# Performance work log

Hardware: AMD Instinct MI355X
Metric: run time of the kernel (lower is better)

Reference implementation:

```python
import jax, jax.numpy as jnp
import numpy as np

DIM = 1024
HEADS = 16
HEAD_DIM = DIM // HEADS
HIDDEN = 4 * DIM
B, N = 4, 2048


def _layernorm(x, g, b, eps=1e-5):
    mu = jnp.mean(x, axis=-1, keepdims=True)
    var = jnp.var(x, axis=-1, keepdims=True)
    return (x - mu) * jax.lax.rsqrt(var + eps) * g + b


def setup_inputs() -> dict:
    key = jax.random.key(0)
    ks = jax.random.split(key, 8)
    s_in = 1.0 / np.sqrt(DIM)
    s_hid = 1.0 / np.sqrt(HIDDEN)
    return {
        "x": jax.random.normal(ks[0], (B, N, DIM), jnp.float32),
        "w_qkv": jax.random.normal(ks[1], (DIM, 3 * DIM), jnp.float32) * s_in,
        "w_proj": jax.random.normal(ks[2], (DIM, DIM), jnp.float32) * s_in,
        "b_proj": jnp.zeros((DIM,), jnp.float32),
        "ln1_g": jnp.ones((DIM,), jnp.float32),
        "ln1_b": jnp.zeros((DIM,), jnp.float32),
        "w1": jax.random.normal(ks[3], (DIM, HIDDEN), jnp.float32) * s_in,
        "b1": jnp.zeros((HIDDEN,), jnp.float32),
        "w2": jax.random.normal(ks[4], (HIDDEN, DIM), jnp.float32) * s_hid,
        "b2": jnp.zeros((DIM,), jnp.float32),
        "ln2_g": jnp.ones((DIM,), jnp.float32),
        "ln2_b": jnp.zeros((DIM,), jnp.float32),
    }


def reference(x, w_qkv, w_proj, b_proj, ln1_g, ln1_b, w1, b1, w2, b2, ln2_g, ln2_b):
    # --- multi-head self-attention (pre-norm), dropout=0 (eval) ---
    h = _layernorm(x, ln1_g, ln1_b)
    qkv = h @ w_qkv                       # [B,N,3*DIM]
    qkv = qkv.reshape(B, N, 3, HEADS, HEAD_DIM)
    q = jnp.transpose(qkv[:, :, 0], (0, 2, 1, 3))  # [B,H,N,hd]
    k = jnp.transpose(qkv[:, :, 1], (0, 2, 1, 3))
    v = jnp.transpose(qkv[:, :, 2], (0, 2, 1, 3))
    scale = HEAD_DIM ** -0.5
    attn = jnp.einsum('bhqd,bhkd->bhqk', q, k) * scale  # [B,H,N,N]
    attn = jax.nn.softmax(attn, axis=-1)
    o = jnp.einsum('bhqk,bhkd->bhqd', attn, v)
    o = jnp.transpose(o, (0, 2, 1, 3)).reshape(B, N, DIM)
    x = o @ w_proj + b_proj + x
    # --- feed-forward (pre-norm), exact GELU ---
    h = _layernorm(x, ln2_g, ln2_b)
    h = jax.nn.gelu(h @ w1 + b1, approximate=False)
    return h @ w2 + b2 + x
```

## Files before the change

### kernel.cpp

```cpp
#include <hip/hip_runtime.h>
#include <cstdint>
#include <cstddef>

typedef float  v4f  __attribute__((ext_vector_type(4)));
typedef __bf16 v8bf __attribute__((ext_vector_type(8)));
typedef __bf16 v4bf __attribute__((ext_vector_type(4)));

__device__ __forceinline__ float b2f(unsigned short u) {
  union { unsigned int i; float f; } cv; cv.i = ((unsigned int)u) << 16; return cv.f;
}
__device__ __forceinline__ unsigned short f2b(float f) {
  union { float f; unsigned int i; } cv; cv.f = f;
  unsigned int i = cv.i;
  i += 0x7fffu + ((i >> 16) & 1u);
  return (unsigned short)(i >> 16);
}
__device__ __forceinline__ unsigned short f2b_trunc(float f) {
  union { float f; unsigned int i; } cv; cv.f = f;
  return (unsigned short)(cv.i >> 16);
}
__device__ __forceinline__ float gelu_fast(float x) {
  const float u = x * (1.5957691216f + 0.07135481627f * x * x);
  return x * (1.0f / (1.0f + __expf(-u)));
}
__device__ __forceinline__ void g2l16(const unsigned short* g, unsigned short* l) {
  __builtin_amdgcn_global_load_lds(
      (const __attribute__((address_space(1))) void*)g,
      (__attribute__((address_space(3))) void*)l,
      16, 0, 0);
}

__global__ __launch_bounds__(256) void transpose_k(const float* __restrict__ in,
                                                   unsigned short* __restrict__ out,
                                                   int R, int C) {
  __shared__ float tile[32][33];
  const int tx = threadIdx.x, ty = threadIdx.y;
  const int r0 = blockIdx.y * 32, c0 = blockIdx.x * 32;
#pragma unroll
  for (int j = 0; j < 4; ++j)
    tile[ty + 8 * j][tx] = in[(size_t)(r0 + ty + 8 * j) * C + c0 + tx];
  __syncthreads();
#pragma unroll
  for (int j = 0; j < 4; ++j)
    out[(size_t)(c0 + ty + 8 * j) * R + r0 + tx] = f2b(tile[tx][ty + 8 * j]);
}

__global__ __launch_bounds__(256) void ln_kernel(const void* __restrict__ xp, int in_bf16,
                                                 const float* __restrict__ g,
                                                 const float* __restrict__ bta,
                                                 unsigned short* __restrict__ out) {
  const int r = blockIdx.x, t = threadIdx.x;
  float v0, v1, v2, v3;
  if (in_bf16) {
    const ushort4 raw = *(const ushort4*)((const unsigned short*)xp + (size_t)r * 1024 + t * 4);
    v0 = b2f(raw.x); v1 = b2f(raw.y); v2 = b2f(raw.z); v3 = b2f(raw.w);
  } else {
    const float4 raw = *(const float4*)((const float*)xp + (size_t)r * 1024 + t * 4);
    v0 = raw.x; v1 = raw.y; v2 = raw.z; v3 = raw.w;
  }
  float s  = v0 + v1 + v2 + v3;
  float s2 = v0 * v0 + v1 * v1 + v2 * v2 + v3 * v3;
#pragma unroll
  for (int off = 32; off > 0; off >>= 1) {
    s  += __shfl_down(s, off);
    s2 += __shfl_down(s2, off);
  }
  __shared__ float red[8];
  const int w = t >> 6, lane = t & 63;
  if (lane == 0) { red[w] = s; red[4 + w] = s2; }
  __syncthreads();
  if (t == 0) {
    float ts = red[0] + red[1] + red[2] + red[3];
    float t2 = red[4] + red[5] + red[6] + red[7];
    float mu = ts * (1.0f / 1024.0f);
    float var = t2 * (1.0f / 1024.0f) - mu * mu;
    red[0] = mu;
    red[1] = rsqrtf(var + 1e-5f);
  }
  __syncthreads();
  const float mu = red[0], rs = red[1];
  const float4 graw = *(const float4*)(g + t * 4);
  const float4 braw = *(const float4*)(bta + t * 4);
  ushort4 o;
  o.x = f2b((v0 - mu) * rs * graw.x + braw.x);
  o.y = f2b((v1 - mu) * rs * graw.y + braw.y);
  o.z = f2b((v2 - mu) * rs * graw.z + braw.z);
  o.w = f2b((v3 - mu) * rs * graw.w + braw.w);
  *(ushort4*)(out + (size_t)r * 1024 + t * 4) = o;
}

__global__ __launch_bounds__(256, 2) void gemm_bt(const unsigned short* __restrict__ A,
                                                  const unsigned short* __restrict__ Bt,
                                                  const float* __restrict__ bias,
                                                  const void* __restrict__ res, int res_bf16,
                                                  void* __restrict__ Cout,
                                                  int M, int N, int K, int act, int out_bf16,
                                                  int swap_xy) {
  __shared__ __align__(16) unsigned short As[3][128 * 32];
  __shared__ __align__(16) unsigned short Bs[3][128 * 32];
  const int t = threadIdx.x;
  const int lane = t & 63, w = t >> 6;
  const int wr = (w >> 1) * 64, wc = (w & 1) * 64;
  const int lr = lane & 15, lq = lane >> 4;
  const int mb = swap_xy ? blockIdx.x : blockIdx.y;
  const int nb = swap_xy ? blockIdx.y : blockIdx.x;
  const int m0 = mb * 128, n0 = nb * 128;

  const int c0 = t, c1 = t + 256;
  const int r0 = c0 >> 2, o0 = (c0 & 3) << 3;
  const int r1 = c1 >> 2, o1 = (c1 & 3) << 3;
  const unsigned short* Ag0 = A  + (size_t)(m0 + r0) * K + o0;
  const unsigned short* Ag1 = A  + (size_t)(m0 + r1) * K + o1;
  const unsigned short* Bg0 = Bt + (size_t)(n0 + r0) * K + o0;
  const unsigned short* Bg1 = Bt + (size_t)(n0 + r1) * K + o1;

  v4f acc[4][4];
#pragma unroll
  for (int mi = 0; mi < 4; ++mi)
#pragma unroll
    for (int ni = 0; ni < 4; ++ni)
      acc[mi][ni] = (v4f){0.f, 0.f, 0.f, 0.f};

  const int nt = K >> 5;
  g2l16(Ag0, &As[0][c0 * 8]); g2l16(Bg0, &Bs[0][c0 * 8]);
  g2l16(Ag1, &As[0][c1 * 8]); g2l16(Bg1, &Bs[0][c1 * 8]);
  if (nt > 1) {
    g2l16(Ag0 + 32, &As[1][c0 * 8]); g2l16(Bg0 + 32, &Bs[1][c0 * 8]);
    g2l16(Ag1 + 32, &As[1][c1 * 8]); g2l16(Bg1 + 32, &Bs[1][c1 * 8]);
  }

  int bi = 0;
  for (int tt = 0; tt < nt; ++tt) {
    const int pf = tt + 2;
    if (pf < nt) {
      const int ko = pf << 5;
      const int pb = pf % 3;
      g2l16(Ag0 + ko, &As[pb][c0 * 8]); g2l16(Bg0 + ko, &Bs[pb][c0 * 8]);
      g2l16(Ag1 + ko, &As[pb][c1 * 8]); g2l16(Bg1 + ko, &Bs[pb][c1 * 8]);
      asm volatile("s_waitcnt vmcnt(8)" ::: "memory");
    } else if (tt + 1 < nt) {
      asm volatile("s_waitcnt vmcnt(4)" ::: "memory");
    } else {
      asm volatile("s_waitcnt vmcnt(0)" ::: "memory");
    }
    __builtin_amdgcn_s_barrier();
    asm volatile("" ::: "memory");

    v8bf af[4], bfr[4];
#pragma unroll
    for (int i = 0; i < 4; ++i) {
      af[i]  = *(const v8bf*)(&As[bi][(wr + i * 16 + lr) * 32 + lq * 8]);
      bfr[i] = *(const v8bf*)(&Bs[bi][(wc + i * 16 + lr) * 32 + lq * 8]);
    }
#pragma unroll
    for (int mi = 0; mi < 4; ++mi)
#pragma unroll
      for (int ni = 0; ni < 4; ++ni)
        acc[mi][ni] = __builtin_amdgcn_mfma_f32_16x16x32_bf16(af[mi], bfr[ni], acc[mi][ni], 0, 0, 0);

    asm volatile("" ::: "memory");
    __builtin_amdgcn_s_barrier();
    bi = (bi == 2) ? 0 : bi + 1;
  }

#pragma unroll
  for (int mi = 0; mi < 4; ++mi) {
#pragma unroll
    for (int ni = 0; ni < 4; ++ni) {
      const int col = n0 + wc + ni * 16 + lr;
      const float bv = bias ? bias[col] : 0.0f;
#pragma unroll
      for (int r = 0; r < 4; ++r) {
        const int row = m0 + wr + mi * 16 + lq * 4 + r;
        float v = acc[mi][ni][r] + bv;
        if (act) v = gelu_fast(v);
        if (res) {
          v += res_bf16 ? b2f(((const unsigned short*)res)[(size_t)row * N + col])
                        : ((const float*)res)[(size_t)row * N + col];
        }
        if (out_bf16)
          ((unsigned short*)Cout)[(size_t)row * N + col] = f2b(v);
        else
          ((float*)Cout)[(size_t)row * N + col] = v;
      }
    }
  }
}

__global__ __launch_bounds__(256) void vt_k(const unsigned short* __restrict__ qkv,
                                            unsigned short* __restrict__ Vt) {
  const int t = threadIdx.x;
  const int n = blockIdx.x * 256 + t, h = blockIdx.y, b = blockIdx.z;
  const size_t src = (size_t)(b * 2048 + n) * 3072 + 2048 + h * 64;
  unsigned short v[64];
#pragma unroll
  for (int j = 0; j < 8; ++j)
    *(uint4*)(v + j * 8) = *(const uint4*)(qkv + src + j * 8);
  const size_t dstbase = ((size_t)(b * 16 + h) * 64) * 2048 + n;
#pragma unroll
  for (int d = 0; d < 64; ++d)
    Vt[dstbase + (size_t)d * 2048] = v[d];
}

__global__ __launch_bounds__(256, 2) void attn_mfma(const unsigned short* __restrict__ qkv,
                                                    const unsigned short* __restrict__ Vt,
                                                    unsigned short* __restrict__ out) {
  __shared__ __align__(16) unsigned short Ks[64 * 80];
  __shared__ __align__(16) unsigned short Vs[64 * 80];
  __shared__ __align__(16) unsigned short Ps[4][32 * 76];
  const int t = threadIdx.x;
  const int lane = t & 63, w = t >> 6;
  const int lr = lane & 15, lq = lane >> 4;
  const int h = blockIdx.x, b = blockIdx.z;
  const int q0 = blockIdx.y * 128 + w * 32;

  v8bf aq[2][2];
#pragma unroll
  for (int mi = 0; mi < 2; ++mi)
#pragma unroll
    for (int kq = 0; kq < 2; ++kq)
      aq[mi][kq] = *(const v8bf*)(qkv + (size_t)(b * 2048 + q0 + mi * 16 + lr) * 3072
                                  + h * 64 + kq * 32 + lq * 8);

  v4f acc_o[2][4];
  float lsum[2][4];
#pragma unroll
  for (int mi = 0; mi < 2; ++mi)
#pragma unroll
    for (int di = 0; di < 4; ++di)
      acc_o[mi][di] = (v4f){0.f, 0.f, 0.f, 0.f};
#pragma unroll
  for (int mi = 0; mi < 2; ++mi)
#pragma unroll
    for (int r = 0; r < 4; ++r)
      lsum[mi][r] = 0.0f;

  const int sc0 = t, sc1 = t + 256;
  const int kr0 = sc0 >> 3, ko0 = (sc0 & 7) * 8;
  const int kr1 = sc1 >> 3, ko1 = (sc1 & 7) * 8;
  const unsigned short* Kg0 = qkv + (size_t)(b * 2048 + kr0) * 3072 + 1024 + h * 64 + ko0;
  const unsigned short* Kg1 = qkv + (size_t)(b * 2048 + kr1) * 3072 + 1024 + h * 64 + ko1;
  const unsigned short* Vg0 = Vt + ((size_t)(b * 16 + h) * 64 + kr0) * 2048 + ko0;
  const unsigned short* Vg1 = Vt + ((size_t)(b * 16 + h) * 64 + kr1) * 2048 + ko1;

  uint4 kreg0 = *(const uint4*)(Kg0);
  uint4 kreg1 = *(const uint4*)(Kg1);
  uint4 vreg0 = *(const uint4*)(Vg0);
  uint4 vreg1 = *(const uint4*)(Vg1);
  *(uint4*)(Ks + kr0 * 80 + ko0) = kreg0;
  *(uint4*)(Ks + kr1 * 80 + ko1) = kreg1;
  *(uint4*)(Vs + kr0 * 80 + ko0) = vreg0;
  *(uint4*)(Vs + kr1 * 80 + ko1) = vreg1;
  __syncthreads();

  for (int kt = 0; kt < 32; ++kt) {
    if (kt < 31) {
      const size_t kn = (size_t)(kt + 1) * 64;
      kreg0 = *(const uint4*)(Kg0 + kn * 3072);
      kreg1 = *(const uint4*)(Kg1 + kn * 3072);
      vreg0 = *(const uint4*)(Vg0 + kn);
      vreg1 = *(const uint4*)(Vg1 + kn);
    }

    v4f s_acc[2][4];
#pragma unroll
    for (int mi = 0; mi < 2; ++mi)
#pragma unroll
      for (int ni = 0; ni < 4; ++ni)
        s_acc[mi][ni] = (v4f){0.f, 0.f, 0.f, 0.f};
#pragma unroll
    for (int kq = 0; kq < 2; ++kq) {
      v8bf bk[4];
#pragma unroll
      for (int ni = 0; ni < 4; ++ni)
        bk[ni] = *(const v8bf*)(Ks + (ni * 16 + lr) * 80 + kq * 32 + lq * 8);
      __builtin_amdgcn_s_setprio(1);
#pragma unroll
      for (int mi = 0; mi < 2; ++mi)
#pragma unroll
        for (int ni = 0; ni < 4; ++ni)
          s_acc[mi][ni] = __builtin_amdgcn_mfma_f32_16x16x32_bf16(aq[mi][kq], bk[ni], s_acc[mi][ni], 0, 0, 0);
      __builtin_amdgcn_s_setprio(0);
    }

#pragma unroll
    for (int mi = 0; mi < 2; ++mi)
#pragma unroll
      for (int ni = 0; ni < 4; ++ni)
#pragma unroll
        for (int r = 0; r < 4; ++r) {
          const float p = __expf(s_acc[mi][ni][r] * 0.125f);
          const unsigned short pb = f2b_trunc(p);
          lsum[mi][r] += b2f(pb);
          Ps[w][(mi * 16 + lq * 4 + r) * 76 + ni * 16 + lr] = pb;
        }

#pragma unroll
    for (int ks = 0; ks < 2; ++ks) {
      v8bf ap[2], bv[4];
#pragma unroll
      for (int mi = 0; mi < 2; ++mi) {
        const unsigned short* base = Ps[w] + (mi * 16 + lr) * 76 + ks * 32 + lq * 8;
        const v4bf lo = *(const v4bf*)(base);
        const v4bf hi = *(const v4bf*)(base + 4);
        ap[mi] = __builtin_shufflevector(lo, hi, 0, 1, 2, 3, 4, 5, 6, 7);
      }
#pragma unroll
      for (int di = 0; di < 4; ++di)
        bv[di] = *(const v8bf*)(Vs + (di * 16 + lr) * 80 + ks * 32 + lq * 8);
      __builtin_amdgcn_s_setprio(1);
#pragma unroll
      for (int mi = 0; mi < 2; ++mi)
#pragma unroll
        for (int di = 0; di < 4; ++di)
          acc_o[mi][di] = __builtin_amdgcn_mfma_f32_16x16x32_bf16(ap[mi], bv[di], acc_o[mi][di], 0, 0, 0);
      __builtin_amdgcn_s_setprio(0);
    }

    __syncthreads();
    if (kt < 31) {
      *(uint4*)(Ks + kr0 * 80 + ko0) = kreg0;
      *(uint4*)(Ks + kr1 * 80 + ko1) = kreg1;
      *(uint4*)(Vs + kr0 * 80 + ko0) = vreg0;
      *(uint4*)(Vs + kr1 * 80 + ko1) = vreg1;
    }
    __syncthreads();
  }

#pragma unroll
  for (int mi = 0; mi < 2; ++mi)
#pragma unroll
    for (int r = 0; r < 4; ++r) {
      float v = lsum[mi][r];
      v += __shfl_xor(v, 1);
      v += __shfl_xor(v, 2);
      v += __shfl_xor(v, 4);
      v += __shfl_xor(v, 8);
      lsum[mi][r] = 1.0f / v;
    }

#pragma unroll
  for (int mi = 0; mi < 2; ++mi)
#pragma unroll
    for (int di = 0; di < 4; ++di)
#pragma unroll
      for (int r = 0; r < 4; ++r)
        out[(size_t)(b * 2048 + q0 + mi * 16 + lq * 4 + r) * 1024 + h * 64 + di * 16 + lr] =
            f2b(acc_o[mi][di][r] * lsum[mi][r]);
}

extern "C" void kernel_launch(void* const* d_in, const int* in_sizes, int n_in,
                              void* d_out, int out_size, void* d_ws, size_t ws_size,
                              hipStream_t stream) {
  (void)in_sizes; (void)n_in; (void)out_size; (void)ws_size;
  const float* x      = (const float*)d_in[0];
  const float* w_qkv  = (const float*)d_in[1];
  const float* w_proj = (const float*)d_in[2];
  const float* b_proj = (const float*)d_in[3];
  const float* ln1_g  = (const float*)d_in[4];
  const float* ln1_b  = (const float*)d_in[5];
  const float* w1     = (const float*)d_in[6];
  const float* b1     = (const float*)d_in[7];
  const float* w2     = (const float*)d_in[8];
  const float* b2     = (const float*)d_in[9];
  const float* ln2_g  = (const float*)d_in[10];
  const float* ln2_b  = (const float*)d_in[11];
  float* out = (float*)d_out;

  char* ws = (char*)d_ws;
  unsigned short* T_a   = (unsigned short*)(ws);
  unsigned short* T_b   = (unsigned short*)(ws + 8388608);
  unsigned short* x2buf = (unsigned short*)(ws + 16777216);
  unsigned short* Vtbuf = (unsigned short*)(ws + 33554432);
  unsigned short* Hbuf  = (unsigned short*)(ws + 50331648);
  unsigned short* qkvb  = (unsigned short*)(ws + 67108864);
  unsigned short* h3buf = (unsigned short*)(ws + 50331648);
  unsigned short* h2buf = (unsigned short*)d_out;

  const dim3 tb(32, 8);
  transpose_k<<<dim3(96, 32),  tb, 0, stream>>>(w_qkv,  T_a, 1024, 3072);
  transpose_k<<<dim3(32, 32),  tb, 0, stream>>>(w_proj, T_b, 1024, 1024);
  ln_kernel<<<8192, 256, 0, stream>>>(x, 0, ln1_g, ln1_b, Hbuf);
  gemm_bt<<<dim3(24, 64), 256, 0, stream>>>(Hbuf, T_a, nullptr, nullptr, 0, qkvb, 8192, 3072, 1024, 0, 1, 0);
  transpose_k<<<dim3(128, 32), tb, 0, stream>>>(w1, T_a, 1024, 4096);
  vt_k<<<dim3(8, 16, 4), 256, 0, stream>>>(qkvb, Vtbuf);
  attn_mfma<<<dim3(16, 16, 4), 256, 0, stream>>>(qkvb, Vtbuf, Hbuf);
  gemm_bt<<<dim3(64, 8), 256, 0, stream>>>(Hbuf, T_b, b_proj, x, 0, x2buf, 8192, 1024, 1024, 0, 1, 1);
  transpose_k<<<dim3(32, 128), tb, 0, stream>>>(w2, T_b, 4096, 1024);
  ln_kernel<<<8192, 256, 0, stream>>>(x2buf, 1, ln2_g, ln2_b, h2buf);
  gemm_bt<<<dim3(32, 64), 256, 0, stream>>>(h2buf, T_a, b1, nullptr, 0, h3buf, 8192, 4096, 1024, 1, 1, 0);
  gemm_bt<<<dim3(64, 8), 256, 0, stream>>>(h3buf, T_b, b2, x2buf, 1, out, 8192, 1024, 4096, 0, 0, 1);
}
```

Before: 583.7 us.

## Swizzle GEMM LDS layout and remap blocks for XCD-aware column-chunk locality

The GEMM now uses a 1D grid. Block IDs are remapped so that consecutive blocks on each of the 8 XCDs walk M-tiles within a narrow chunk of N-columns (NBC wide), with the aim of improving L2 reuse of the B operand per XCD. Separately, the LDS tile layout is XOR-swizzled on the 16-byte column groups at both global-to-LDS write and fragment read, to reduce LDS bank conflicts. The mapping assumes the grid size is divisible by 8 and M is a multiple of 128.

```diff
diff --git a/kernel.cpp b/kernel.cpp
--- a/kernel.cpp
+++ b/kernel.cpp
@@ -95,24 +95,34 @@
                                                   const void* __restrict__ res, int res_bf16,
                                                   void* __restrict__ Cout,
                                                   int M, int N, int K, int act, int out_bf16,
-                                                  int swap_xy) {
+                                                  int NBC) {
   __shared__ __align__(16) unsigned short As[3][128 * 32];
   __shared__ __align__(16) unsigned short Bs[3][128 * 32];
   const int t = threadIdx.x;
   const int lane = t & 63, w = t >> 6;
   const int wr = (w >> 1) * 64, wc = (w & 1) * 64;
   const int lr = lane & 15, lq = lane >> 4;
-  const int mb = swap_xy ? blockIdx.x : blockIdx.y;
-  const int nb = swap_xy ? blockIdx.y : blockIdx.x;
+
+  const int nwg = gridDim.x;
+  const int bid = blockIdx.x;
+  const int q8 = nwg >> 3;
+  const int r = (bid & 7) * q8 + (bid >> 3);
+  const int MBt = M >> 7;
+  const int chunkW = MBt * NBC;
+  const int c = r / chunkW, ci = r - c * chunkW;
+  const int mb = ci / NBC;
+  const int nb = c * NBC + (ci - (ci / NBC) * NBC);
   const int m0 = mb * 128, n0 = nb * 128;
 
   const int c0 = t, c1 = t + 256;
-  const int r0 = c0 >> 2, o0 = (c0 & 3) << 3;
-  const int r1 = c1 >> 2, o1 = (c1 & 3) << 3;
+  const int r0 = c0 >> 2, o0 = (((c0 & 3) ^ ((c0 >> 3) & 3)) << 3);
+  const int r1 = c1 >> 2, o1 = (((c1 & 3) ^ ((c1 >> 3) & 3)) << 3);
   const unsigned short* Ag0 = A  + (size_t)(m0 + r0) * K + o0;
   const unsigned short* Ag1 = A  + (size_t)(m0 + r1) * K + o1;
   const unsigned short* Bg0 = Bt + (size_t)(n0 + r0) * K + o0;
   const unsigned short* Bg1 = Bt + (size_t)(n0 + r1) * K + o1;
+
+  const int ra = ((lq ^ ((lr >> 1) & 3)) << 3);
 
   v4f acc[4][4];
 #pragma unroll
@@ -149,8 +159,8 @@
     v8bf af[4], bfr[4];
 #pragma unroll
     for (int i = 0; i < 4; ++i) {
-      af[i]  = *(const v8bf*)(&As[bi][(wr + i * 16 + lr) * 32 + lq * 8]);
-      bfr[i] = *(const v8bf*)(&Bs[bi][(wc + i * 16 + lr) * 32 + lq * 8]);
+      af[i]  = *(const v8bf*)(&As[bi][(wr + i * 16 + lr) * 32 + ra]);
+      bfr[i] = *(const v8bf*)(&Bs[bi][(wc + i * 16 + lr) * 32 + ra]);
     }
 #pragma unroll
     for (int mi = 0; mi < 4; ++mi)
@@ -170,9 +180,9 @@
       const int col = n0 + wc + ni * 16 + lr;
       const float bv = bias ? bias[col] : 0.0f;
 #pragma unroll
-      for (int r = 0; r < 4; ++r) {
-        const int row = m0 + wr + mi * 16 + lq * 4 + r;
-        float v = acc[mi][ni][r] + bv;
+      for (int rr = 0; rr < 4; ++rr) {
+        const int row = m0 + wr + mi * 16 + lq * 4 + rr;
+        float v = acc[mi][ni][rr] + bv;
         if (act) v = gelu_fast(v);
         if (res) {
           v += res_bf16 ? b2f(((const unsigned short*)res)[(size_t)row * N + col])
@@ -381,13 +391,13 @@
   transpose_k<<<dim3(96, 32),  tb, 0, stream>>>(w_qkv,  T_a, 1024, 3072);
   transpose_k<<<dim3(32, 32),  tb, 0, stream>>>(w_proj, T_b, 1024, 1024);
   ln_kernel<<<8192, 256, 0, stream>>>(x, 0, ln1_g, ln1_b, Hbuf);
-  gemm_bt<<<dim3(24, 64), 256, 0, stream>>>(Hbuf, T_a, nullptr, nullptr, 0, qkvb, 8192, 3072, 1024, 0, 1, 0);
+  gemm_bt<<<1536, 256, 0, stream>>>(Hbuf, T_a, nullptr, nullptr, 0, qkvb, 8192, 3072, 1024, 0, 1, 3);
   transpose_k<<<dim3(128, 32), tb, 0, stream>>>(w1, T_a, 1024, 4096);
   vt_k<<<dim3(8, 16, 4), 256, 0, stream>>>(qkvb, Vtbuf);
   attn_mfma<<<dim3(16, 16, 4), 256, 0, stream>>>(qkvb, Vtbuf, Hbuf);
-  gemm_bt<<<dim3(64, 8), 256, 0, stream>>>(Hbuf, T_b, b_proj, x, 0, x2buf, 8192, 1024, 1024, 0, 1, 1);
+  gemm_bt<<<512, 256, 0, stream>>>(Hbuf, T_b, b_proj, x, 0, x2buf, 8192, 1024, 1024, 0, 1, 1);
   transpose_k<<<dim3(32, 128), tb, 0, stream>>>(w2, T_b, 4096, 1024);
   ln_kernel<<<8192, 256, 0, stream>>>(x2buf, 1, ln2_g, ln2_b, h2buf);
-  gemm_bt<<<dim3(32, 64), 256, 0, stream>>>(h2buf, T_a, b1, nullptr, 0, h3buf, 8192, 4096, 1024, 1, 1, 0);
-  gemm_bt<<<dim3(64, 8), 256, 0, stream>>>(h3buf, T_b, b2, x2buf, 1, out, 8192, 1024, 4096, 0, 0, 1);
-}
+  gemm_bt<<<2048, 256, 0, stream>>>(h2buf, T_a, b1, nullptr, 0, h3buf, 8192, 4096, 1024, 1, 1, 4);
+  gemm_bt<<<512, 256, 0, stream>>>(h3buf, T_b, b2, x2buf, 1, out, 8192, 1024, 4096, 0, 0, 1);
+}
```

Result: slower. 599.4 us (+2.7%).
